# Kernel optimization log

Measured on AMD Instinct MI355X. Metric: run time of the kernel, lower is better.

## Reference

```python
import jax, jax.numpy as jnp
import numpy as np

# libmolgrid GridMaker defaults (gnina): resolution 0.5 A, dimension 23.5 A
RES = 0.5
DIM = 23.5
G = int(round(DIM / RES)) + 1  # 48 grid points per axis
N_ATOMS = 800
N_TYPES = 28  # gnina default atom typing


def setup_inputs() -> dict:
    key = jax.random.key(0)
    k1, k2, k3 = jax.random.split(key, 3)
    # atoms spread around the grid center (grid spans +-11.75 A)
    coords = jax.random.normal(k1, (N_ATOMS, 3), dtype=jnp.float32) * 4.0
    # continuous (soft) type vectors in [0,1)
    types = jax.random.uniform(k2, (N_ATOMS, N_TYPES), dtype=jnp.float32)
    # van-der-Waals-like radii in [1.0, 1.8) A
    radii = 1.0 + 0.8 * jax.random.uniform(k3, (N_ATOMS,), dtype=jnp.float32)
    center = jnp.zeros((3,), dtype=jnp.float32)
    return {"center": center, "coords": coords, "types": types, "radii": radii}


def _density(coords, radii, center):
    """Per-atom libmolgrid density on the [G,G,G] grid -> [N,G,G,G].

    f(d) = exp(-2 d^2/r^2)                         for d <  r
         = e^-2 (4 (d/r)^2 - 12 (d/r) + 9)          for r <= d < 1.5 r
         = 0                                        otherwise
    (C1-continuous quadratic tail, libmolgrid defaults grm=1.0, final=1.5).
    """
    origin = center - DIM / 2.0  # [3]
    ax = jnp.arange(G, dtype=jnp.float32) * RES  # [G]
    dx = (origin[0] + ax)[None, :] - coords[:, 0:1]  # [N,G]
    dy = (origin[1] + ax)[None, :] - coords[:, 1:2]
    dz = (origin[2] + ax)[None, :] - coords[:, 2:3]
    d2 = (dx[:, :, None, None] ** 2
          + dy[:, None, :, None] ** 2
          + dz[:, None, None, :] ** 2)  # [N,G,G,G]
    r = radii[:, None, None, None]
    dr2 = d2 / (r * r)
    dr = jnp.sqrt(jnp.maximum(dr2, 1e-12))
    gauss = jnp.exp(-2.0 * dr2)
    inv_e2 = jnp.float32(np.exp(-2.0))
    quad = inv_e2 * (4.0 * dr2 - 12.0 * dr + 9.0)
    return jnp.where(dr < 1.0, gauss, jnp.where(dr < 1.5, quad, 0.0))


def reference(center, coords, types, radii):
    dens = _density(coords, radii, center)  # [N,G,G,G]
    # weight each atom's footprint by its type vector and scatter-sum over atoms
    return jnp.einsum('nxyz,nt->txyz', dens, types)  # [T,G,G,G]
```

## Files before the change

### kernel.cpp

```cpp
#include <hip/hip_runtime.h>

#define GR    48
#define GR3   (GR * GR * GR)
#define NA    800
#define NT    28
#define RESF  0.5f
#define HALF_DIM 11.75f
#define INV_E2 0.13533528323661270f
#define TILE  4
#define NTPD  (GR / TILE)
#define NBLK  (NTPD * NTPD * NTPD)
#define KB    64
#define TPW   (NT / 4)

__global__ __launch_bounds__(256) void c2g_kernel(
    const float* __restrict__ center,
    const float* __restrict__ coords,
    const float* __restrict__ types,
    const float* __restrict__ radii,
    float* __restrict__ out)
{
    __shared__ float s_ax[NA], s_ay[NA], s_az[NA], s_ir2[NA];
    __shared__ int   s_ai[NA];
    __shared__ int   s_cnt;
    __shared__ float s_val[KB * 64];

    const int tid  = threadIdx.x;
    const int lane = tid & 63;
    const int w    = tid >> 6;
    const int b    = blockIdx.x;
    const int tz   = b % NTPD;
    const int ty   = (b / NTPD) % NTPD;
    const int tx   = b / (NTPD * NTPD);

    const float ox = center[0] - HALF_DIM;
    const float oy = center[1] - HALF_DIM;
    const float oz = center[2] - HALF_DIM;

    const float bxlo = ox + tx * (TILE * RESF), bxhi = bxlo + (TILE - 1) * RESF;
    const float bylo = oy + ty * (TILE * RESF), byhi = bylo + (TILE - 1) * RESF;
    const float bzlo = oz + tz * (TILE * RESF), bzhi = bzlo + (TILE - 1) * RESF;

    if (tid == 0) s_cnt = 0;
    __syncthreads();

    for (int a0 = 0; a0 < NA; a0 += 256) {
        int a = a0 + tid;
        bool accept = false;
        float ax = 0.f, ay = 0.f, az = 0.f, r = 1.f;
        if (a < NA) {
            ax = coords[3 * a + 0];
            ay = coords[3 * a + 1];
            az = coords[3 * a + 2];
            r  = radii[a];
            float cut = 1.5f * r;
            float ddx = ax - fminf(fmaxf(ax, bxlo), bxhi);
            float ddy = ay - fminf(fmaxf(ay, bylo), byhi);
            float ddz = az - fminf(fmaxf(az, bzlo), bzhi);
            float d2 = fmaf(ddx, ddx, fmaf(ddy, ddy, ddz * ddz));
            accept = d2 < cut * cut;
        }
        unsigned long long m = __ballot(accept);
        if (m) {
            int base = 0;
            if (lane == 0) base = atomicAdd(&s_cnt, __popcll(m));
            base = __shfl(base, 0);
            if (accept) {
                int p = base + __popcll(m & ((1ull << lane) - 1ull));
                s_ax[p] = ax; s_ay[p] = ay; s_az[p] = az;
                s_ir2[p] = 1.0f / (r * r);
                s_ai[p] = a;
            }
        }
    }
    __syncthreads();
    const int cnt = s_cnt;

    const int lz = lane & 3;
    const int ly = (lane >> 2) & 3;
    const int lx = lane >> 4;
    const float gx = bxlo + lx * RESF;
    const float gy = bylo + ly * RESF;
    const float gz = bzlo + lz * RESF;

    float acc[TPW];
    #pragma unroll
    for (int j = 0; j < TPW; ++j) acc[j] = 0.0f;
    const int tbase = w * TPW;

    for (int k0 = 0; k0 < cnt; k0 += KB) {
        #pragma unroll
        for (int j = 0; j < 16; ++j) {
            int row = w * 16 + j;
            int k = k0 + row;
            float val = 0.0f;
            if (k < cnt) {
                float dx = gx - s_ax[k];
                float dy = gy - s_ay[k];
                float dz = gz - s_az[k];
                float d2 = fmaf(dx, dx, fmaf(dy, dy, dz * dz));
                float dr2 = d2 * s_ir2[k];
                float g  = __expf(-2.0f * dr2);
                float dr = sqrtf(dr2);
                float q  = INV_E2 * fmaf(4.0f, dr2, fmaf(-12.0f, dr, 9.0f));
                val = (dr2 < 1.0f) ? g : ((dr2 < 2.25f) ? q : 0.0f);
            }
            s_val[row * 64 + lane] = val;
        }
        __syncthreads();

        const int kmax = (cnt - k0 < KB) ? (cnt - k0) : KB;
        #pragma unroll 4
        for (int k = 0; k < kmax; ++k) {
            float v = s_val[k * 64 + lane];
            int a = __builtin_amdgcn_readfirstlane(s_ai[k0 + k]);
            const float* trow = types + a * NT + tbase;
            #pragma unroll
            for (int j = 0; j < TPW; ++j)
                acc[j] = fmaf(v, trow[j], acc[j]);
        }
        __syncthreads();
    }

    const int gidx = ((tx * TILE + lx) * GR + (ty * TILE + ly)) * GR + tz * TILE + lz;
    #pragma unroll
    for (int j = 0; j < TPW; ++j)
        out[(tbase + j) * GR3 + gidx] = acc[j];
}

extern "C" void kernel_launch(void* const* d_in, const int* in_sizes, int n_in,
                              void* d_out, int out_size, void* d_ws, size_t ws_size,
                              hipStream_t stream) {
    const float* center = (const float*)d_in[0];
    const float* coords = (const float*)d_in[1];
    const float* types  = (const float*)d_in[2];
    const float* radii  = (const float*)d_in[3];
    float* out = (float*)d_out;

    c2g_kernel<<<dim3(NBLK), dim3(256), 0, stream>>>(center, coords, types, radii, out);
}
```

Measured before the change: 86.56 us.

## Stage type rows in shared memory and use 2x2x16 tiles for coalesced stores

The per-block tile changes from 4x4x4 to 2x2x16, so each wavefront writes 16 contiguous z elements and output stores coalesce better. For each chunk of 64 atoms, the type vectors are loaded cooperatively into shared memory with float4 loads, replacing per-lane scalar global loads in the inner loop. Each wave now handles 8 type slots, padded to 32, so the last wave does some wasted FMAs. The block's bounding box is also more elongated, which can raise the accepted-atom count per block.

```diff
diff --git a/kernel.cpp b/kernel.cpp
--- a/kernel.cpp
+++ b/kernel.cpp
@@ -1,17 +1,23 @@
 #include <hip/hip_runtime.h>
 
 #define GR    48
+#define GR2   (GR * GR)
 #define GR3   (GR * GR * GR)
 #define NA    800
 #define NT    28
 #define RESF  0.5f
 #define HALF_DIM 11.75f
 #define INV_E2 0.13533528323661270f
-#define TILE  4
-#define NTPD  (GR / TILE)
-#define NBLK  (NTPD * NTPD * NTPD)
+
+#define TXC   2
+#define TYC   2
+#define TZC   16
+#define NTX   (GR / TXC)
+#define NTY   (GR / TYC)
+#define NTZ   (GR / TZC)
+#define NBLK  (NTX * NTY * NTZ)
 #define KB    64
-#define TPW   (NT / 4)
+#define TSL   8
 
 __global__ __launch_bounds__(256) void c2g_kernel(
     const float* __restrict__ center,
@@ -24,22 +30,23 @@
     __shared__ int   s_ai[NA];
     __shared__ int   s_cnt;
     __shared__ float s_val[KB * 64];
+    __shared__ float s_tb[KB * 32];
 
     const int tid  = threadIdx.x;
     const int lane = tid & 63;
     const int w    = tid >> 6;
     const int b    = blockIdx.x;
-    const int tz   = b % NTPD;
-    const int ty   = (b / NTPD) % NTPD;
-    const int tx   = b / (NTPD * NTPD);
+    const int tz   = b % NTZ;
+    const int ty   = (b / NTZ) % NTY;
+    const int tx   = b / (NTZ * NTY);
 
     const float ox = center[0] - HALF_DIM;
     const float oy = center[1] - HALF_DIM;
     const float oz = center[2] - HALF_DIM;
 
-    const float bxlo = ox + tx * (TILE * RESF), bxhi = bxlo + (TILE - 1) * RESF;
-    const float bylo = oy + ty * (TILE * RESF), byhi = bylo + (TILE - 1) * RESF;
-    const float bzlo = oz + tz * (TILE * RESF), bzhi = bzlo + (TILE - 1) * RESF;
+    const float bxlo = ox + tx * (TXC * RESF), bxhi = bxlo + (TXC - 1) * RESF;
+    const float bylo = oy + ty * (TYC * RESF), byhi = bylo + (TYC - 1) * RESF;
+    const float bzlo = oz + tz * (TZC * RESF), bzhi = bzlo + (TZC - 1) * RESF;
 
     if (tid == 0) s_cnt = 0;
     __syncthreads();
@@ -76,25 +83,40 @@
     __syncthreads();
     const int cnt = s_cnt;
 
-    const int lz = lane & 3;
-    const int ly = (lane >> 2) & 3;
-    const int lx = lane >> 4;
-    const float gx = bxlo + lx * RESF;
-    const float gy = bylo + ly * RESF;
-    const float gz = bzlo + lz * RESF;
+    const int lzz = lane & 15;
+    const int ly2 = (lane >> 4) & 1;
+    const int lx2 = lane >> 5;
+    const float gx = bxlo + lx2 * RESF;
+    const float gy = bylo + ly2 * RESF;
+    const float gz = bzlo + lzz * RESF;
 
-    float acc[TPW];
+    float acc[TSL];
     #pragma unroll
-    for (int j = 0; j < TPW; ++j) acc[j] = 0.0f;
-    const int tbase = w * TPW;
+    for (int j = 0; j < TSL; ++j) acc[j] = 0.0f;
+    const int tbase = w * TSL;
 
     for (int k0 = 0; k0 < cnt; k0 += KB) {
+        const int kmax = (cnt - k0 < KB) ? (cnt - k0) : KB;
+
+        float4 tv0 = make_float4(0.f, 0.f, 0.f, 0.f);
+        float4 tv1 = tv0;
+        {
+            int s = tid;
+            int row = s >> 3, q = s & 7;
+            if (q < 7 && row < kmax)
+                tv0 = *(const float4*)(types + s_ai[k0 + row] * NT + q * 4);
+            s = tid + 256;
+            row = s >> 3; q = s & 7;
+            if (q < 7 && row < kmax)
+                tv1 = *(const float4*)(types + s_ai[k0 + row] * NT + q * 4);
+        }
+
         #pragma unroll
         for (int j = 0; j < 16; ++j) {
             int row = w * 16 + j;
-            int k = k0 + row;
             float val = 0.0f;
-            if (k < cnt) {
+            if (row < kmax) {
+                int k = k0 + row;
                 float dx = gx - s_ax[k];
                 float dy = gy - s_ay[k];
                 float dz = gz - s_az[k];
@@ -107,25 +129,32 @@
             }
             s_val[row * 64 + lane] = val;
         }
+
+        {
+            int s = tid;
+            *(float4*)&s_tb[(s >> 3) * 32 + (s & 7) * 4] = tv0;
+            s = tid + 256;
+            *(float4*)&s_tb[(s >> 3) * 32 + (s & 7) * 4] = tv1;
+        }
         __syncthreads();
 
-        const int kmax = (cnt - k0 < KB) ? (cnt - k0) : KB;
         #pragma unroll 4
         for (int k = 0; k < kmax; ++k) {
             float v = s_val[k * 64 + lane];
-            int a = __builtin_amdgcn_readfirstlane(s_ai[k0 + k]);
-            const float* trow = types + a * NT + tbase;
+            const float* tr = &s_tb[k * 32 + tbase];
             #pragma unroll
-            for (int j = 0; j < TPW; ++j)
-                acc[j] = fmaf(v, trow[j], acc[j]);
+            for (int j = 0; j < TSL; ++j)
+                acc[j] = fmaf(v, tr[j], acc[j]);
         }
         __syncthreads();
     }
 
-    const int gidx = ((tx * TILE + lx) * GR + (ty * TILE + ly)) * GR + tz * TILE + lz;
+    const int gidx = (tx * TXC + lx2) * GR2 + (ty * TYC + ly2) * GR + tz * TZC + lzz;
     #pragma unroll
-    for (int j = 0; j < TPW; ++j)
-        out[(tbase + j) * GR3 + gidx] = acc[j];
+    for (int j = 0; j < TSL; ++j) {
+        int t = tbase + j;
+        if (t < NT) out[t * GR3 + gidx] = acc[j];
+    }
 }
 
 extern "C" void kernel_launch(void* const* d_in, const int* in_sizes, int n_in,
```

New measurement: 74.40 us. 1.16x faster.
